# Kernel optimization log

Measured on AMD Instinct MI355X. Metric: run time of the kernel, lower is better.

The kernel has to match this reference:

```python
import jax, jax.numpy as jnp
import numpy as np

B = 256      # batch
C = 512      # num_classes (independent heads)
F = 768      # BERT pooler_output dim (hard-coded in module)
D = 512      # dense_layer_size


def setup_inputs() -> dict:
    key = jax.random.key(0)
    ks = jax.random.split(key, 7)
    s1 = 1.0 / np.sqrt(F)
    s2 = 1.0 / np.sqrt(D)
    return {
        "x":  jax.random.normal(ks[0], (B, F), dtype=jnp.float32),
        "W1": jax.random.normal(ks[1], (C, F, D), dtype=jnp.float32) * s1,
        "b1": jax.random.normal(ks[2], (C, D), dtype=jnp.float32) * s1,
        "W2": jax.random.normal(ks[3], (C, D, D), dtype=jnp.float32) * s2,
        "b2": jax.random.normal(ks[4], (C, D), dtype=jnp.float32) * s2,
        "W3": jax.random.normal(ks[5], (C, D, 2), dtype=jnp.float32) * s2,
        "b3": jax.random.normal(ks[6], (C, 2), dtype=jnp.float32) * s2,
    }


def reference(x, W1, b1, W2, b2, W3, b3):
    # Batched version of the per-class Python loop:
    # each head: Linear(F,D)-ReLU-(Dropout=identity in eval)-Linear(D,D)-ReLU-Linear(D,2)
    h = jax.nn.relu(jnp.einsum('bf,cfd->bcd', x, W1) + b1[None])        # [B, C, D]
    h = jax.nn.relu(jnp.einsum('bcd,cde->bce', h, W2) + b2[None])        # [B, C, D]
    out = jnp.einsum('bcd,cde->bce', h, W3) + b3[None]                   # [B, C, 2]
    return out
```

## Files before the change

kernel.cpp:

```cpp
#include <hip/hip_runtime.h>
#include <stdint.h>

typedef float f32x4 __attribute__((ext_vector_type(4)));
typedef float f32x2 __attribute__((ext_vector_type(2)));
typedef short bf16x8 __attribute__((ext_vector_type(8)));
typedef uint32_t u32x4 __attribute__((ext_vector_type(4)));

__device__ __forceinline__ uint32_t bf16_rne(float f) {
  uint32_t x = __float_as_uint(f);
  return (x + 0x7FFFu + ((x >> 16) & 1u)) >> 16;
}

__device__ __forceinline__ void load_lds_16B(void* lds_dst, const void* gsrc) {
  __builtin_amdgcn_global_load_lds(
      (const __attribute__((address_space(1))) unsigned int*)gsrc,
      (__attribute__((address_space(3))) unsigned int*)lds_dst, 16, 0, 0);
}

__global__ void cast_x_kernel(const float* __restrict__ x,
                              uint32_t* __restrict__ xb, int n2) {
  int i = blockIdx.x * 256 + threadIdx.x;
  if (i >= n2) return;
  f32x2 v = *(const f32x2*)(x + 2 * i);
  xb[i] = bf16_rne(v[0]) | (bf16_rne(v[1]) << 16);
}

template <int K, int MODE>
__global__ __launch_bounds__(512, 4) void gemm_fused(
    const uint16_t* __restrict__ Abase, long long aClassStride,
    const float* __restrict__ Wbase, const float* __restrict__ biasBase,
    uint16_t* __restrict__ Hout, const float* __restrict__ W3base,
    float* __restrict__ part) {
  constexpr int NT = K / 64;
  __shared__ uint8_t smem[81920];

  const int tid = threadIdx.x;
  const int bid = blockIdx.x;
  const int logical = ((bid & 7) << 9) | (bid >> 3);
  const int c = logical >> 3;
  const int nt = logical & 7;
  const int n0 = nt * 64;

  const uint16_t* Ab = Abase + (size_t)c * (size_t)aClassStride;
  const float* Wc = Wbase + (size_t)c * (K * 512) + n0;

  const int l = tid & 63, w = tid >> 6;
  const int lr = l & 15, lg = l >> 4;

  f32x4 acc[2][4];
#pragma unroll
  for (int i = 0; i < 2; i++)
#pragma unroll
    for (int j = 0; j < 4; j++) acc[i][j] = {0.f, 0.f, 0.f, 0.f};

  auto stageA = [&](int ts, int buf) {
    uint8_t* base = smem + buf * 40960;
    const uint16_t* As = Ab + ts * 64;
#pragma unroll
    for (int i = 0; i < 4; i++) {
      int idx = tid + i * 512;
      int m = idx >> 3, cc = idx & 7;
      int ccs = cc ^ (m & 7);
      load_lds_16B(base + ((w * 64 + i * 512) << 4),
                   As + (size_t)m * K + ccs * 8);
    }
  };
  auto loadB = [&](int ts, float* g) {
    const float* Ws = Wc + (size_t)(ts * 64 + w * 8) * 512 + l;
#pragma unroll
    for (int r = 0; r < 8; r++) g[r] = Ws[(size_t)r * 512];
  };
  auto writeB = [&](const float* g, int buf) {
    u32x4 p;
#pragma unroll
    for (int j = 0; j < 4; j++)
      p[j] = bf16_rne(g[2 * j]) | (bf16_rne(g[2 * j + 1]) << 16);
    *(u32x4*)(smem + buf * 40960 + 32768 + l * 128 + ((w ^ (l & 7)) << 4)) = p;
  };
  auto comp = [&](int buf) {
    const uint8_t* s = smem + buf * 40960;
#pragma unroll
    for (int kk = 0; kk < 2; ++kk) {
      const int kx = ((lg * 16) ^ ((lr & 7) << 4)) ^ (kk << 6);
      bf16x8 a[2], b[4];
#pragma unroll
      for (int mf = 0; mf < 2; mf++)
        a[mf] = *(const bf16x8*)(s + (w * 32 + mf * 16 + lr) * 128 + kx);
#pragma unroll
      for (int nf = 0; nf < 4; nf++)
        b[nf] = *(const bf16x8*)(s + 32768 + (nf * 16 + lr) * 128 + kx);
#pragma unroll
      for (int mf = 0; mf < 2; mf++)
#pragma unroll
        for (int nf = 0; nf < 4; nf++)
          acc[mf][nf] = __builtin_amdgcn_mfma_f32_16x16x32_bf16(
              a[mf], b[nf], acc[mf][nf], 0, 0, 0);
    }
  };

  float g0[8], g1[8];
  stageA(0, 0);
  loadB(0, g0);
  writeB(g0, 0);
  __syncthreads();
  stageA(1, 1);
  loadB(1, g1);

#pragma unroll 1
  for (int t = 0; t < NT; t += 2) {
    comp(0);
    writeB(g1, 1);
    __syncthreads();
    if (t + 2 < NT) { stageA(t + 2, 0); loadB(t + 2, g0); }
    comp(1);
    if (t + 2 < NT) {
      writeB(g0, 0);
      __syncthreads();
      if (t + 3 < NT) { stageA(t + 3, 1); loadB(t + 3, g1); }
    }
  }

  float bv[4];
#pragma unroll
  for (int nf = 0; nf < 4; nf++)
    bv[nf] = biasBase[c * 512 + n0 + nf * 16 + lr];

  if constexpr (MODE == 0) {
    uint16_t* Oc = Hout + (size_t)c * 131072 + n0;
#pragma unroll
    for (int mf = 0; mf < 2; mf++)
#pragma unroll
      for (int nf = 0; nf < 4; nf++)
#pragma unroll
        for (int r = 0; r < 4; r++) {
          int m = w * 32 + mf * 16 + lg * 4 + r;
          float v = fmaxf(acc[mf][nf][r] + bv[nf], 0.f);
          Oc[(size_t)m * 512 + nf * 16 + lr] = (uint16_t)bf16_rne(v);
        }
  } else {
    float w30[4], w31[4];
#pragma unroll
    for (int nf = 0; nf < 4; nf++) {
      f32x2 t = *(const f32x2*)(W3base +
                                ((size_t)c * 512 + n0 + nf * 16 + lr) * 2);
      w30[nf] = t[0];
      w31[nf] = t[1];
    }
#pragma unroll
    for (int mf = 0; mf < 2; mf++)
#pragma unroll
      for (int r = 0; r < 4; r++) {
        float s0 = 0.f, s1 = 0.f;
#pragma unroll
        for (int nf = 0; nf < 4; nf++) {
          float v = fmaxf(acc[mf][nf][r] + bv[nf], 0.f);
          s0 += v * w30[nf];
          s1 += v * w31[nf];
        }
#pragma unroll
        for (int d = 1; d < 16; d <<= 1) {
          s0 += __shfl_xor(s0, d);
          s1 += __shfl_xor(s1, d);
        }
        if (lr == 0) {
          int m = w * 32 + mf * 16 + lg * 4 + r;
          *(f32x2*)(part + (((size_t)c * 256 + m) * 8 + nt) * 2) =
              f32x2{s0, s1};
        }
      }
  }
}

__global__ __launch_bounds__(512) void reduce_out(
    const float* __restrict__ part, const float* __restrict__ b3,
    float* __restrict__ out) {
  const int b = blockIdx.x, c = threadIdx.x;
  const f32x4* p = (const f32x4*)(part + ((size_t)c * 256 + b) * 16);
  f32x4 v0 = p[0], v1 = p[1], v2 = p[2], v3 = p[3];
  float s0 = b3[c * 2] + v0[0] + v0[2] + v1[0] + v1[2] + v2[0] + v2[2] +
             v3[0] + v3[2];
  float s1 = b3[c * 2 + 1] + v0[1] + v0[3] + v1[1] + v1[3] + v2[1] + v2[3] +
             v3[1] + v3[3];
  *(f32x2*)(out + ((size_t)b * 512 + c) * 2) = f32x2{s0, s1};
}

extern "C" void kernel_launch(void* const* d_in, const int* in_sizes, int n_in,
                              void* d_out, int out_size, void* d_ws,
                              size_t ws_size, hipStream_t stream) {
  const float* x = (const float*)d_in[0];
  const float* W1 = (const float*)d_in[1];
  const float* b1 = (const float*)d_in[2];
  const float* W2 = (const float*)d_in[3];
  const float* b2 = (const float*)d_in[4];
  const float* W3 = (const float*)d_in[5];
  const float* b3 = (const float*)d_in[6];
  float* out = (float*)d_out;

  uint8_t* ws = (uint8_t*)d_ws;
  const size_t xb_off = 0;
  const size_t h1_off = 393216;
  const size_t part_off = h1_off + 134217728;
  const size_t need = part_off + 8388608;
  if (ws_size < need) return;

  uint32_t* xb = (uint32_t*)(ws + xb_off);
  uint16_t* h1 = (uint16_t*)(ws + h1_off);
  float* part = (float*)(ws + part_off);

  cast_x_kernel<<<dim3(384), dim3(256), 0, stream>>>(x, xb, 98304);
  gemm_fused<768, 0><<<dim3(4096), dim3(512), 0, stream>>>(
      (const uint16_t*)xb, 0LL, W1, b1, h1, nullptr, nullptr);
  gemm_fused<512, 1><<<dim3(4096), dim3(512), 0, stream>>>(
      h1, 131072LL, W2, b2, nullptr, W3, part);
  reduce_out<<<dim3(256), dim3(512), 0, stream>>>(part, b3, out);
}
```

Baseline: 408.7 us.

## Load A operand directly from global into registers, shrink LDS to B only

Removes LDS staging of the activation (A) tile and instead has each lane read its MFMA A fragments directly from global memory inside the compute step. LDS usage drops from 80KB to 16KB, which should allow more resident blocks to overlap the streaming of fp32 weights. Barriers are replaced with a lighter lgkmcnt wait plus s_barrier, and weight prefetch loads are issued earlier. The risk is exposed global/L2 latency on the A loads, since they are no longer prefetched ahead of use.

```diff
diff --git a/kernel.cpp b/kernel.cpp
--- a/kernel.cpp
+++ b/kernel.cpp
@@ -11,10 +11,8 @@
   return (x + 0x7FFFu + ((x >> 16) & 1u)) >> 16;
 }
 
-__device__ __forceinline__ void load_lds_16B(void* lds_dst, const void* gsrc) {
-  __builtin_amdgcn_global_load_lds(
-      (const __attribute__((address_space(1))) unsigned int*)gsrc,
-      (__attribute__((address_space(3))) unsigned int*)lds_dst, 16, 0, 0);
+__device__ __forceinline__ void ldsbar() {
+  asm volatile("s_waitcnt lgkmcnt(0)\n\ts_barrier" ::: "memory");
 }
 
 __global__ void cast_x_kernel(const float* __restrict__ x,
@@ -32,7 +30,7 @@
     uint16_t* __restrict__ Hout, const float* __restrict__ W3base,
     float* __restrict__ part) {
   constexpr int NT = K / 64;
-  __shared__ uint8_t smem[81920];
+  __shared__ uint8_t smem[16384];
 
   const int tid = threadIdx.x;
   const int bid = blockIdx.x;
@@ -47,24 +45,14 @@
   const int l = tid & 63, w = tid >> 6;
   const int lr = l & 15, lg = l >> 4;
 
+  const uint16_t* Ap = Ab + (size_t)(w * 32 + lr) * K + lg * 8;
+
   f32x4 acc[2][4];
 #pragma unroll
   for (int i = 0; i < 2; i++)
 #pragma unroll
     for (int j = 0; j < 4; j++) acc[i][j] = {0.f, 0.f, 0.f, 0.f};
 
-  auto stageA = [&](int ts, int buf) {
-    uint8_t* base = smem + buf * 40960;
-    const uint16_t* As = Ab + ts * 64;
-#pragma unroll
-    for (int i = 0; i < 4; i++) {
-      int idx = tid + i * 512;
-      int m = idx >> 3, cc = idx & 7;
-      int ccs = cc ^ (m & 7);
-      load_lds_16B(base + ((w * 64 + i * 512) << 4),
-                   As + (size_t)m * K + ccs * 8);
-    }
-  };
   auto loadB = [&](int ts, float* g) {
     const float* Ws = Wc + (size_t)(ts * 64 + w * 8) * 512 + l;
 #pragma unroll
@@ -75,48 +63,50 @@
 #pragma unroll
     for (int j = 0; j < 4; j++)
       p[j] = bf16_rne(g[2 * j]) | (bf16_rne(g[2 * j + 1]) << 16);
-    *(u32x4*)(smem + buf * 40960 + 32768 + l * 128 + ((w ^ (l & 7)) << 4)) = p;
+    *(u32x4*)(smem + buf * 8192 + l * 128 + ((w ^ (l & 7)) << 4)) = p;
   };
-  auto comp = [&](int buf) {
-    const uint8_t* s = smem + buf * 40960;
+  auto comp = [&](int buf, int t) {
+    const uint8_t* s = smem + buf * 8192;
+    bf16x8 a[4];
+#pragma unroll
+    for (int kk = 0; kk < 2; ++kk)
+#pragma unroll
+      for (int mf = 0; mf < 2; mf++)
+        a[kk * 2 + mf] =
+            *(const bf16x8*)(Ap + t * 64 + kk * 32 + (size_t)mf * 16 * K);
 #pragma unroll
     for (int kk = 0; kk < 2; ++kk) {
       const int kx = ((lg * 16) ^ ((lr & 7) << 4)) ^ (kk << 6);
-      bf16x8 a[2], b[4];
-#pragma unroll
-      for (int mf = 0; mf < 2; mf++)
-        a[mf] = *(const bf16x8*)(s + (w * 32 + mf * 16 + lr) * 128 + kx);
+      bf16x8 b[4];
 #pragma unroll
       for (int nf = 0; nf < 4; nf++)
-        b[nf] = *(const bf16x8*)(s + 32768 + (nf * 16 + lr) * 128 + kx);
+        b[nf] = *(const bf16x8*)(s + (nf * 16 + lr) * 128 + kx);
 #pragma unroll
       for (int mf = 0; mf < 2; mf++)
 #pragma unroll
         for (int nf = 0; nf < 4; nf++)
           acc[mf][nf] = __builtin_amdgcn_mfma_f32_16x16x32_bf16(
-              a[mf], b[nf], acc[mf][nf], 0, 0, 0);
+              a[kk * 2 + mf], b[nf], acc[mf][nf], 0, 0, 0);
     }
   };
 
   float g0[8], g1[8];
-  stageA(0, 0);
   loadB(0, g0);
+  loadB(1, g1);
   writeB(g0, 0);
-  __syncthreads();
-  stageA(1, 1);
-  loadB(1, g1);
+  ldsbar();
 
 #pragma unroll 1
   for (int t = 0; t < NT; t += 2) {
-    comp(0);
+    comp(0, t);
+    if (t + 2 < NT) loadB(t + 2, g0);
     writeB(g1, 1);
-    __syncthreads();
-    if (t + 2 < NT) { stageA(t + 2, 0); loadB(t + 2, g0); }
-    comp(1);
+    ldsbar();
+    comp(1, t + 1);
+    if (t + 3 < NT) loadB(t + 3, g1);
     if (t + 2 < NT) {
       writeB(g0, 0);
-      __syncthreads();
-      if (t + 3 < NT) { stageA(t + 3, 1); loadB(t + 3, g1); }
+      ldsbar();
     }
   }
 
```

Result: slower. 482.5 us (+18.1%).
